# Kernel optimization log

Hardware: AMD Instinct MI355X
Metric: run time of the kernel (lower is better)

## Reference

```python
import jax, jax.numpy as jnp
import numpy as np
import math

B, T = 2, 1024
D_MODEL = 1024
N_HEAD = 16
HEAD_DIM = D_MODEL // N_HEAD
VOCAB = 32000
NUM_LOOP = 4
EPS_LN = 1e-5                       # torch LayerNorm default
EPS_RMS = float(np.finfo(np.float32).eps)  # torch RMSNorm eps=None -> finfo eps


def setup_inputs() -> dict:
    key = jax.random.key(0)
    ks = jax.random.split(key, 12)
    s = 0.02
    d = D_MODEL
    tok = jax.random.normal(ks[1], (VOCAB, d), jnp.float32) * s
    tok = tok.at[0].set(0.0)  # padding_idx=0
    return {
        "idx": jax.random.randint(ks[0], (B, T), 0, VOCAB),
        "tok_embed": tok,
        "ln_e_g": jnp.ones((d,), jnp.float32),
        "ln_e_b": jnp.zeros((d,), jnp.float32),
        "Wqkv": jax.random.normal(ks[2], (d, 3 * d), jnp.float32) * s,
        "bqkv": jnp.zeros((3 * d,), jnp.float32),
        "Wo": jax.random.normal(ks[3], (d, d), jnp.float32) * s,
        "bo": jnp.zeros((d,), jnp.float32),
        "W1": jax.random.normal(ks[4], (d, 4 * d), jnp.float32) * s,
        "b1": jnp.zeros((4 * d,), jnp.float32),
        "W2": jax.random.normal(ks[5], (4 * d, d), jnp.float32) * s,
        "b2": jnp.zeros((d,), jnp.float32),
        "n1_w": jnp.ones((d,), jnp.float32),
        "n2_w": jnp.ones((d,), jnp.float32),
        "lnf_g": jnp.ones((d,), jnp.float32),
        "lnf_b": jnp.zeros((d,), jnp.float32),
        "Wlm": jax.random.normal(ks[6], (d, VOCAB), jnp.float32) * s,
        "blm": jnp.zeros((VOCAB,), jnp.float32),
    }


def layernorm(x, g, b):
    m = jnp.mean(x, axis=-1, keepdims=True)
    v = jnp.mean(jnp.square(x - m), axis=-1, keepdims=True)
    return (x - m) * jax.lax.rsqrt(v + EPS_LN) * g + b


def rmsnorm(x, w):
    ms = jnp.mean(jnp.square(x), axis=-1, keepdims=True)
    return x * jax.lax.rsqrt(ms + EPS_RMS) * w


def gelu_tanh(x):
    c = math.sqrt(2.0 / math.pi)
    return 0.5 * x * (1.0 + jnp.tanh(c * (x + 0.044715 * x * x * x)))


def alibi_causal_bias(t):
    # rpe[q,k] = -(q-k) for q>k else 0, scaled per head by 2^(-8/H*(h+1)); causal -inf above diag
    pos = jnp.arange(t)
    rel = pos[:, None] - pos[None, :]                      # [T,T] = q - k
    slopes = 2.0 ** (-8.0 / N_HEAD * jnp.arange(1, N_HEAD + 1, dtype=jnp.float32))
    bias = -slopes[:, None, None] * rel.astype(jnp.float32)  # [H,T,T]
    return jnp.where(rel[None] >= 0, bias, -jnp.inf)       # causal mask fused


def reference(idx, tok_embed, ln_e_g, ln_e_b, Wqkv, bqkv, Wo, bo,
              W1, b1, W2, b2, n1_w, n2_w, lnf_g, lnf_b, Wlm, blm):
    b, t = idx.shape
    x = layernorm(tok_embed[idx], ln_e_g, ln_e_b)          # rpe=True: no sinusoidal PE
    bias = alibi_causal_bias(t)                            # [H,T,T]
    scale = 1.0 / math.sqrt(HEAD_DIM)

    for _ in range(NUM_LOOP):
        # attention sublayer
        h = rmsnorm(x, n1_w)
        qkv = h @ Wqkv + bqkv
        q, k, v = jnp.split(qkv, 3, axis=-1)
        q = q.reshape(b, t, N_HEAD, HEAD_DIM).transpose(0, 2, 1, 3)
        k = k.reshape(b, t, N_HEAD, HEAD_DIM).transpose(0, 2, 1, 3)
        v = v.reshape(b, t, N_HEAD, HEAD_DIM).transpose(0, 2, 1, 3)
        att = jnp.einsum('bhqd,bhkd->bhqk', q, k) * scale + bias[None]
        att = jax.nn.softmax(att, axis=-1)
        y = jnp.einsum('bhqk,bhkd->bhqd', att, v)
        y = y.transpose(0, 2, 1, 3).reshape(b, t, D_MODEL)
        x = x + (y @ Wo + bo)
        # mlp sublayer
        h = rmsnorm(x, n2_w)
        x = x + (gelu_tanh(h @ W1 + b1) @ W2 + b2)

    x = layernorm(x, lnf_g, lnf_b)
    return x @ Wlm + blm  # [B,T,VOCAB]
```

## Files before the change

### kernel.cpp

```cpp
#include <hip/hip_runtime.h>
#include <stdint.h>

#define DEVI __device__ __forceinline__

typedef __attribute__((ext_vector_type(8))) short short8;
typedef __attribute__((ext_vector_type(4))) float f32x4;
typedef unsigned short u16;
typedef unsigned int u32;

typedef const __attribute__((address_space(1))) void* gas_ptr;
typedef __attribute__((address_space(3))) void* las_ptr;

constexpr int BBATCH = 2;
constexpr int TT  = 1024;
constexpr int BT  = BBATCH * TT;
constexpr int DM  = 1024;
constexpr int NH  = 16;
constexpr int HD  = 64;
constexpr int DFF = 4096;
constexpr int NV  = 32000;
constexpr int NL  = 4;

DEVI u16 f2b(float f) {
  u32 u = __builtin_bit_cast(u32, f);
  u = (u + 0x7fffu + ((u >> 16) & 1u)) >> 16;
  return (u16)u;
}
DEVI float b2f(u16 h) { return __builtin_bit_cast(float, (u32)h << 16); }

DEVI void gld16(const void* g, void* l) {
  __builtin_amdgcn_global_load_lds((gas_ptr)g, (las_ptr)l, 16, 0, 0);
}

DEVI float wave_sum(float v) {
#pragma unroll
  for (int off = 32; off; off >>= 1) v += __shfl_xor(v, off);
  return v;
}
DEVI float block_sum(float v, float* sb) {
  v = wave_sum(v);
  int lane = threadIdx.x & 63, wid = threadIdx.x >> 6;
  __syncthreads();
  if (lane == 0) sb[wid] = v;
  __syncthreads();
  return sb[0] + sb[1] + sb[2] + sb[3];
}

DEVI float gelu_f(float x) {
  float u = 0.7978845608028654f * (x + 0.044715f * x * x * x);
  float e = __expf(2.0f * u);
  return x * (1.0f - 1.0f / (e + 1.0f));
}

__global__ __launch_bounds__(256) void wt_transpose_all(
    const float* __restrict__ Wqkv, const float* __restrict__ Wo,
    const float* __restrict__ W1, const float* __restrict__ W2,
    const float* __restrict__ Wlm,
    u16* __restrict__ WqkvT, u16* __restrict__ WoT, u16* __restrict__ W1T,
    u16* __restrict__ W2T, u16* __restrict__ WlmT) {
  __shared__ float t[32][33];
  int bid = blockIdx.x;
  const float* in; u16* out; int K, N, tt;
  if (bid < 3072)       { in = Wqkv; out = WqkvT; K = 1024; N = 3072;  tt = bid; }
  else if (bid < 4096)  { in = Wo;   out = WoT;   K = 1024; N = 1024;  tt = bid - 3072; }
  else if (bid < 8192)  { in = W1;   out = W1T;   K = 1024; N = 4096;  tt = bid - 4096; }
  else if (bid < 12288) { in = W2;   out = W2T;   K = 4096; N = 1024;  tt = bid - 8192; }
  else                  { in = Wlm;  out = WlmT;  K = 1024; N = 32000; tt = bid - 12288; }
  int nx = N >> 5;
  int n0 = (tt % nx) * 32, k0 = (tt / nx) * 32;
  int tx = threadIdx.x & 31, ty = threadIdx.x >> 5;
#pragma unroll
  for (int i = 0; i < 4; ++i)
    t[ty + 8 * i][tx] = in[(size_t)(k0 + ty + 8 * i) * N + n0 + tx];
  __syncthreads();
#pragma unroll
  for (int i = 0; i < 4; ++i)
    out[(size_t)(n0 + ty + 8 * i) * K + k0 + tx] = f2b(t[tx][ty + 8 * i]);
}

__global__ __launch_bounds__(256) void embed_ln_k(const int* __restrict__ idx,
                                                  const float* __restrict__ tok,
                                                  const float* __restrict__ g,
                                                  const float* __restrict__ b,
                                                  float* __restrict__ x) {
  __shared__ float sb[4];
  int row = blockIdx.x, tid = threadIdx.x;
  float4 v = ((const float4*)(tok + (size_t)idx[row] * DM))[tid];
  float s = block_sum(v.x + v.y + v.z + v.w, sb);
  float m = s * (1.0f / DM);
  float dx = v.x - m, dy = v.y - m, dz = v.z - m, dw = v.w - m;
  float q = block_sum(dx * dx + dy * dy + dz * dz + dw * dw, sb);
  float rs = rsqrtf(q * (1.0f / DM) + 1e-5f);
  float4 gg = ((const float4*)g)[tid];
  float4 bb = ((const float4*)b)[tid];
  float4 o = make_float4(dx * rs * gg.x + bb.x, dy * rs * gg.y + bb.y,
                         dz * rs * gg.z + bb.z, dw * rs * gg.w + bb.w);
  ((float4*)(x + (size_t)row * DM))[tid] = o;
}

__global__ __launch_bounds__(256) void final_ln_k(const float* __restrict__ x,
                                                  const float* __restrict__ g,
                                                  const float* __restrict__ b,
                                                  u16* __restrict__ xf) {
  __shared__ float sb[4];
  int row = blockIdx.x, tid = threadIdx.x;
  float4 v = ((const float4*)(x + (size_t)row * DM))[tid];
  float s = block_sum(v.x + v.y + v.z + v.w, sb);
  float m = s * (1.0f / DM);
  float dx = v.x - m, dy = v.y - m, dz = v.z - m, dw = v.w - m;
  float q = block_sum(dx * dx + dy * dy + dz * dz + dw * dw, sb);
  float rs = rsqrtf(q * (1.0f / DM) + 1e-5f);
  float4 gg = ((const float4*)g)[tid];
  float4 bb = ((const float4*)b)[tid];
  u32 lo = (u32)f2b(dx * rs * gg.x + bb.x) | ((u32)f2b(dy * rs * gg.y + bb.y) << 16);
  u32 hi = (u32)f2b(dz * rs * gg.z + bb.z) | ((u32)f2b(dw * rs * gg.w + bb.w) << 16);
  ((uint2*)(xf + (size_t)row * DM))[tid] = make_uint2(lo, hi);
}

__global__ __launch_bounds__(256) void rmsnorm_k(const float* __restrict__ x,
                                                 const float* __restrict__ w,
                                                 u16* __restrict__ h) {
  __shared__ float sb[4];
  int row = blockIdx.x, tid = threadIdx.x;
  float4 v = ((const float4*)(x + (size_t)row * DM))[tid];
  float q = block_sum(v.x * v.x + v.y * v.y + v.z * v.z + v.w * v.w, sb);
  float rs = rsqrtf(q * (1.0f / DM) + 1.1920928955078125e-7f);
  float4 ww = ((const float4*)w)[tid];
  u32 lo = (u32)f2b(v.x * rs * ww.x) | ((u32)f2b(v.y * rs * ww.y) << 16);
  u32 hi = (u32)f2b(v.z * rs * ww.z) | ((u32)f2b(v.w * rs * ww.w) << 16);
  ((uint2*)(h + (size_t)row * DM))[tid] = make_uint2(lo, hi);
}

__global__ __launch_bounds__(256) void attn_k(const u16* __restrict__ qkv,
                                              const u16* __restrict__ vT,
                                              u16* __restrict__ y) {
  __shared__ __align__(16) char sP[16384];
  __shared__ __align__(16) char sK[16384];
  __shared__ __align__(16) char sV[16384];
  const int tid = threadIdx.x, lane = tid & 63, wid = tid >> 6;
  const int bid = blockIdx.x;
  const int sl = (bid + (bid >> 8)) & 15;
  const int qt = (sl & 1) ? (sl >> 1) : (15 - (sl >> 1));
  const int bh = (bid >> 4) & 31, b = bh >> 4, h = bh & 15;
  const int nt = (qt >> 1) + 1;
  const float slope = exp2f(-0.5f * (float)(h + 1));

  const char* Qb = (const char*)(qkv + (size_t)b * TT * 3 * DM + h * HD);
  const char* Kb = (const char*)(qkv + (size_t)b * TT * 3 * DM + DM + h * HD);
  const char* Vb = (const char*)(vT + (size_t)bh * HD * TT);

#pragma unroll
  for (int ci = 0; ci < 2; ++ci) {
    int c = wid * 2 + ci;
    int r = c * 8 + (lane >> 3);
    int q = (lane & 7) ^ (r & 7);
    gld16(Qb + (size_t)(qt * 64 + r) * 6144 + q * 16, sP + c * 1024 + lane * 16);
  }

  auto stageKV = [&](int kt) {
    int kv0 = kt * 128;
#pragma unroll
    for (int ci = 0; ci < 4; ++ci) {
      int c = wid * 4 + ci;
      int r = c * 8 + (lane >> 3);
      int q = (lane & 7) ^ (r & 7);
      gld16(Kb + (size_t)(kv0 + r) * 6144 + q * 16, sK + c * 1024 + lane * 16);
    }
#pragma unroll
    for (int ci = 0; ci < 4; ++ci) {
      int c = wid * 4 + ci;
      int d = c * 4 + (lane >> 4);
      int q = (lane & 15) ^ (d & 15);
      gld16(Vb + (size_t)d * 2048 + (size_t)kv0 * 2 + q * 16, sV + c * 1024 + lane * 16);
    }
  };
  stageKV(0);
  asm volatile("s_waitcnt vmcnt(8)" ::: "memory");

  short8 qf[2];
#pragma unroll
  for (int ks = 0; ks < 2; ++ks) {
    int r = wid * 16 + (lane & 15);
    int q = ((ks << 2) + (lane >> 4)) ^ (r & 7);
    qf[ks] = *(const short8*)(sP + r * 128 + q * 16);
  }

  f32x4 Y[4] = {};
  float m_r[4], l_r[4];
#pragma unroll
  for (int r = 0; r < 4; ++r) { m_r[r] = -3e38f; l_r[r] = 0.0f; }

  for (int kt = 0; kt < nt; ++kt) {
    asm volatile("s_waitcnt vmcnt(0)" ::: "memory");
    __syncthreads();

    f32x4 s[8] = {};
    __builtin_amdgcn_s_setprio(1);
#pragma unroll
    for (int ks = 0; ks < 2; ++ks) {
      short8 kf[8];
#pragma unroll
      for (int j = 0; j < 8; ++j) {
        int r = j * 16 + (lane & 15);
        int q = ((ks << 2) + (lane >> 4)) ^ (r & 7);
        kf[j] = *(const short8*)(sK + r * 128 + q * 16);
      }
#pragma unroll
      for (int j = 0; j < 8; ++j)
        s[j] = __builtin_amdgcn_mfma_f32_16x16x32_bf16(qf[ks], kf[j], s[j], 0, 0, 0);
    }
    __builtin_amdgcn_s_setprio(0);

    const int kv0 = kt * 128;
    const int qbase = qt * 64 + wid * 16 + ((lane >> 4) << 2);
    float rowmax[4] = {-3e38f, -3e38f, -3e38f, -3e38f};
#pragma unroll
    for (int j = 0; j < 8; ++j) {
      int kcol = kv0 + j * 16 + (lane & 15);
#pragma unroll
      for (int r = 0; r < 4; ++r) {
        int qrow = qbase + r;
        float v = (kcol <= qrow) ? s[j][r] * 0.125f - slope * (float)(qrow - kcol) : -3e38f;
        s[j][r] = v;
        rowmax[r] = fmaxf(rowmax[r], v);
      }
    }
#pragma unroll
    for (int r = 0; r < 4; ++r) {
      rowmax[r] = fmaxf(rowmax[r], __shfl_xor(rowmax[r], 1));
      rowmax[r] = fmaxf(rowmax[r], __shfl_xor(rowmax[r], 2));
      rowmax[r] = fmaxf(rowmax[r], __shfl_xor(rowmax[r], 4));
      rowmax[r] = fmaxf(rowmax[r], __shfl_xor(rowmax[r], 8));
      float mn = fmaxf(m_r[r], rowmax[r]);
      float al = __expf(m_r[r] - mn);
      m_r[r] = mn;
      l_r[r] *= al;
#pragma unroll
      for (int j = 0; j < 4; ++j) Y[j][r] *= al;
    }
    float rs[4] = {0.0f, 0.0f, 0.0f, 0.0f};
#pragma unroll
    for (int j = 0; j < 8; ++j)
#pragma unroll
      for (int r = 0; r < 4; ++r) {
        float p = __expf(s[j][r] - m_r[r]);
        s[j][r] = p;
        rs[r] += p;
      }
#pragma unroll
    for (int r = 0; r < 4; ++r) {
      rs[r] += __shfl_xor(rs[r], 1);
      rs[r] += __shfl_xor(rs[r], 2);
      rs[r] += __shfl_xor(rs[r], 4);
      rs[r] += __shfl_xor(rs[r], 8);
      l_r[r] += rs[r];
    }
#pragma unroll
    for (int j = 0; j < 8; ++j)
#pragma unroll
      for (int r = 0; r < 4; ++r) {
        int rl = wid * 16 + ((lane >> 4) << 2) + r;
        int c = j * 16 + (lane & 15);
        int g = c >> 3;
        *(u16*)(sP + rl * 256 + ((g ^ (rl & 15)) << 4) + (c & 7) * 2) = f2b(s[j][r]);
      }

    __builtin_amdgcn_s_setprio(1);
#pragma unroll
    for (int ks = 0; ks < 4; ++ks) {
      short8 pf, vf[4];
      {
        int r = wid * 16 + (lane & 15);
        int q = ((ks << 2) + (lane >> 4)) ^ (r & 15);
        pf = *(const short8*)(sP + r * 256 + (q << 4));
      }
#pragma unroll
      for (int j = 0; j < 4; ++j) {
        int d = j * 16 + (lane & 15);
        int q = ((ks << 2) + (lane >> 4)) ^ (d & 15);
        vf[j] = *(const short8*)(sV + d * 256 + (q << 4));
      }
#pragma unroll
      for (int j = 0; j < 4; ++j)
        Y[j] = __builtin_amdgcn_mfma_f32_16x16x32_bf16(pf, vf[j], Y[j], 0, 0, 0);
    }
    __builtin_amdgcn_s_setprio(0);
    __syncthreads();
    if (kt + 1 < nt) stageKV(kt + 1);
  }

#pragma unroll
  for (int r = 0; r < 4; ++r) {
    float inv = 1.0f / l_r[r];
    int qrow = qt * 64 + wid * 16 + ((lane >> 4) << 2) + r;
    u16* yp = y + (size_t)(b * TT + qrow) * DM + h * HD;
#pragma unroll
    for (int j = 0; j < 4; ++j)
      yp[j * 16 + (lane & 15)] = f2b(Y[j][r] * inv);
  }
}

enum { EPI_BF16 = 0, EPI_GELU = 1, EPI_ADDF32 = 2, EPI_F32 = 3, EPI_ATOMIC = 4, EPI_QKV = 5 };

template <int BM, int BN, int WM, int WN, int EPI, int KS = 1>
__global__ __launch_bounds__(256, 2) void gemm_bt(
    const u16* __restrict__ A, int lda, const u16* __restrict__ Bt, int ldb,
    const float* __restrict__ bias, void* __restrict__ C, int ldc,
    float* __restrict__ resid, int K, u16* __restrict__ vTout) {
  constexpr int BK = 64;
  constexpr int NW = WM * WN;
  constexpr int FM = BM / WM / 16, FN = BN / WN / 16;
  constexpr int ABYTES = BM * BK * 2, BBYTES = BN * BK * 2;
  constexpr int ACH = ABYTES / 1024, BCH = BBYTES / 1024, NCH = ACH + BCH;
  extern __shared__ __align__(16) char smem[];

  const int tid = threadIdx.x, lane = tid & 63, wid = tid >> 6;
  const int brow = blockIdx.y * BM, bcol = blockIdx.x * BN;
  const long long kbase2 = (long long)blockIdx.z * (K / KS) * 2;

  const int nt = (K / KS) >> 6;
  const int widm = wid / WN, widn = wid % WN;
  const int rm0 = widm * (BM / WM), cn0 = widn * (BN / WN);

  f32x4 acc[FM][FN] = {};

  const int swq16 = (((lane & 7) ^ ((lane >> 3) & 7)) << 4);
  const int lrow8 = lane >> 3;

  auto stage = [&](int buf, int kt) {
    char* base = smem + buf * (ABYTES + BBYTES);
    const char* Ag = (const char*)A;
    const char* Bg = (const char*)Bt;
    long long kOff = kbase2 + (long long)kt * 128 + swq16;
#pragma unroll
    for (int ci = 0; ci < NCH / NW; ++ci) {
      int c = wid + ci * NW;
      if (c < ACH) {
        int r = c * 8 + lrow8;
        gld16(Ag + (long long)(brow + r) * (lda * 2) + kOff, base + c * 1024 + lane * 16);
      } else {
        int r = (c - ACH) * 8 + lrow8;
        gld16(Bg + (long long)(bcol + r) * (ldb * 2) + kOff,
              base + ABYTES + (c - ACH) * 1024 + lane * 16);
      }
    }
  };

  auto compute = [&](int buf) {
    char* baseA = smem + buf * (ABYTES + BBYTES);
    char* baseB = baseA + ABYTES;
#pragma unroll
    for (int ks = 0; ks < 2; ++ks) {
      short8 af[FM], bv[FN];
#pragma unroll
      for (int i = 0; i < FM; ++i) {
        int r = rm0 + i * 16 + (lane & 15);
        int cq = ((ks << 2) + (lane >> 4)) ^ (r & 7);
        af[i] = *(const short8*)(baseA + r * 128 + (cq << 4));
      }
#pragma unroll
      for (int j = 0; j < FN; ++j) {
        int r = cn0 + j * 16 + (lane & 15);
        int cq = ((ks << 2) + (lane >> 4)) ^ (r & 7);
        bv[j] = *(const short8*)(baseB + r * 128 + (cq << 4));
      }
#pragma unroll
      for (int i = 0; i < FM; ++i)
#pragma unroll
        for (int j = 0; j < FN; ++j)
          acc[i][j] = __builtin_amdgcn_mfma_f32_16x16x32_bf16(af[i], bv[j], acc[i][j], 0, 0, 0);
    }
  };

  stage(0, 0);
  __syncthreads();
  int cur = 0;
  for (int t = 0; t < nt; ++t) {
    if (t + 1 < nt) stage(cur ^ 1, t + 1);
    compute(cur);
    __syncthreads();
    cur ^= 1;
  }

  if constexpr (EPI == EPI_QKV) {
    if (bcol >= 2 * DM) {
      u16* st = (u16*)smem;
#pragma unroll
      for (int i = 0; i < FM; ++i)
#pragma unroll
        for (int j = 0; j < FN; ++j)
#pragma unroll
          for (int r = 0; r < 4; ++r) {
            int rl = rm0 + i * 16 + ((lane >> 4) << 2) + r;
            int cl = cn0 + j * 16 + (lane & 15);
            st[rl * 130 + cl] = f2b(acc[i][j][r] + bias[bcol + cl]);
          }
      __syncthreads();
      const int b = brow >> 10, t0b = brow & (TT - 1);
      const int h0 = (bcol - 2 * DM) >> 6;
      const int sub = tid & 15;
#pragma unroll
      for (int pass = 0; pass < 8; ++pass) {
        int d = pass * 16 + (tid >> 4);
        u32 pk[4];
#pragma unroll
        for (int k2 = 0; k2 < 4; ++k2) {
          u16 lo = st[(sub * 8 + 2 * k2) * 130 + d];
          u16 hi = st[(sub * 8 + 2 * k2 + 1) * 130 + d];
          pk[k2] = (u32)lo | ((u32)hi << 16);
        }
        int head = h0 + (d >> 6), dd = d & 63;
        *(uint4*)(vTout + ((size_t)((b * NH + head) * HD + dd)) * TT + t0b + sub * 8) =
            make_uint4(pk[0], pk[1], pk[2], pk[3]);
      }
      return;
    }
  }

  const int r0 = brow + rm0 + ((lane >> 4) << 2);
  const int c0 = bcol + cn0 + (lane & 15);
#pragma unroll
  for (int i = 0; i < FM; ++i) {
#pragma unroll
    for (int j = 0; j < FN; ++j) {
#pragma unroll
      for (int r = 0; r < 4; ++r) {
        int row = r0 + i * 16 + r;
        int col = c0 + j * 16;
        float v = acc[i][j][r];
        if constexpr (EPI == EPI_BF16 || EPI == EPI_QKV) {
          ((u16*)C)[(size_t)row * ldc + col] = f2b(v + bias[col]);
        } else if constexpr (EPI == EPI_GELU) {
          ((u16*)C)[(size_t)row * ldc + col] = f2b(gelu_f(v + bias[col]));
        } else if constexpr (EPI == EPI_ADDF32) {
          size_t o = (size_t)row * ldc + col;
          resid[o] += v + bias[col];
        } else if constexpr (EPI == EPI_ATOMIC) {
          size_t o = (size_t)row * ldc + col;
          atomicAdd(&resid[o], v + (blockIdx.z == 0 ? bias[col] : 0.0f));
        } else {
          ((float*)C)[(size_t)row * ldc + col] = v + bias[col];
        }
      }
    }
  }
}

template <int EPI>
__global__ __launch_bounds__(512, 2) void gemm8(
    const u16* __restrict__ A, int lda, const u16* __restrict__ Bt, int ldb,
    const float* __restrict__ bias, void* __restrict__ C, int ldc, int K, int nby) {
  __shared__ __align__(16) char smem[2][2][32768];
  const int tid = threadIdx.x, lane = tid & 63;
  const int wid = tid >> 6, wm = wid >> 2, wn = wid & 3;

  const int nb = gridDim.x;
  const int q8 = nb >> 3, r8 = nb & 7;
  const int xcd = blockIdx.x & 7, lin = blockIdx.x >> 3;
  const int idx = (xcd < r8 ? xcd * (q8 + 1) : r8 * (q8 + 1) + (xcd - r8) * q8) + lin;
  const int brow = (idx % nby) * 256, bcol = (idx / nby) * 256;

  const int nt = K >> 6, niter = nt >> 1;

  const int srow = tid >> 3, sq = tid & 7;
  auto stage = [&](int buf, int isB, int half, int kt) {
    const u16* G = isB ? Bt : A;
    const int ld = isB ? ldb : lda;
    const int base = isB ? bcol : brow;
    char* L = &smem[buf][isB][half * 16384];
#pragma unroll
    for (int l = 0; l < 2; ++l) {
      int rl = half * 128 + l * 64 + srow;
      gld16((const char*)G + (size_t)(base + rl) * (ld * 2) + kt * 128 + ((sq ^ (rl & 7)) << 4),
            L + l * 8192 + tid * 16);
    }
  };

  short8 bfr[4][2], afr[2][2];
  f32x4 acc[8][4] = {};

  stage(0, 0, 0, 0); stage(0, 0, 1, 0);
  stage(0, 1, 0, 0); stage(0, 1, 1, 0);
  stage(1, 1, 0, 1); stage(1, 1, 1, 1);
  asm volatile("s_waitcnt vmcnt(0)" ::: "memory");
  __builtin_amdgcn_s_barrier();

  for (int i = 0; i < niter; ++i) {
    const bool full = (i + 1 < niter);
    const int t2 = 2 * i + 2, t3 = 2 * i + 3;
#pragma unroll
    for (int h = 0; h < 2; ++h) {
#pragma unroll
      for (int qd = 0; qd < 4; ++qd) {
        if (qd == 0) {
#pragma unroll
          for (int j = 0; j < 4; ++j)
#pragma unroll
            for (int ks = 0; ks < 2; ++ks) {
              int r = wn * 64 + j * 16 + (lane & 15);
              int q = ((ks << 2) + (lane >> 4)) ^ (r & 7);
              bfr[j][ks] = *(const short8*)&smem[h][1][r * 128 + q * 16];
            }
        }
#pragma unroll
        for (int f = 0; f < 2; ++f)
#pragma unroll
          for (int ks = 0; ks < 2; ++ks) {
            int r = wm * 128 + (qd * 2 + f) * 16 + (lane & 15);
            int q = ((ks << 2) + (lane >> 4)) ^ (r & 7);
            afr[f][ks] = *(const short8*)&smem[h][0][r * 128 + q * 16];
          }
        if (h == 0) {
          if (qd == 0) stage(1, 0, 0, 2 * i + 1);
          else if (qd == 1) stage(1, 0, 1, 2 * i + 1);
          else if (qd == 2) { if (full) stage(0, 1, 0, t2); }
          else              { if (full) stage(0, 1, 1, t2); }
        } else {
          if (qd == 0)      { if (full) stage(0, 0, 0, t2); }
          else if (qd == 1) { if (full) stage(0, 0, 1, t2); }
          else if (qd == 2) { if (full) stage(1, 1, 0, t3); }
          else              { if (full) stage(1, 1, 1, t3); }
        }
        if (qd == 3) {
          if (full) asm volatile("s_waitcnt vmcnt(4)" ::: "memory");
          else if (h == 0) asm volatile("s_waitcnt vmcnt(0)" ::: "memory");
        }
        __builtin_amdgcn_s_barrier();
        asm volatile("s_waitcnt lgkmcnt(0)" ::: "memory");
        __builtin_amdgcn_s_setprio(1);
#pragma unroll
        for (int f = 0; f < 2; ++f)
#pragma unroll
          for (int j = 0; j < 4; ++j)
#pragma unroll
            for (int ks = 0; ks < 2; ++ks)
              acc[qd * 2 + f][j] = __builtin_amdgcn_mfma_f32_16x16x32_bf16(
                  afr[f][ks], bfr[j][ks], acc[qd * 2 + f][j], 0, 0, 0);
        __builtin_amdgcn_s_setprio(0);
        __builtin_amdgcn_s_barrier();
      }
    }
  }

  if constexpr (EPI == EPI_F32) {
    char* sf = &smem[0][0][0];
    float* C32 = (float*)C;
#pragma unroll
    for (int half = 0; half < 2; ++half) {
      if (wm == half) {
#pragma unroll
        for (int fi = 0; fi < 8; ++fi)
#pragma unroll
          for (int j = 0; j < 4; ++j) {
            int cl = wn * 64 + j * 16 + (lane & 15);
            float bv = bias[bcol + cl];
            int qsw = (cl >> 2);
#pragma unroll
            for (int r = 0; r < 4; ++r) {
              int row = fi * 16 + ((lane >> 4) << 2) + r;
              *(float*)(sf + row * 1024 + ((qsw ^ (row & 7)) << 4) + (cl & 3) * 4) =
                  acc[fi][j][r] + bv;
            }
          }
      }
      __syncthreads();
#pragma unroll
      for (int pass = 0; pass < 16; ++pass) {
        int row = pass * 8 + wid;
        float4 v4 = *(float4*)(sf + row * 1024 + ((lane ^ (row & 7)) << 4));
        *(float4*)(C32 + (size_t)(brow + half * 128 + row) * ldc + bcol + lane * 4) = v4;
      }
      __syncthreads();
    }
    return;
  }

  const int r0 = brow + wm * 128 + ((lane >> 4) << 2);
  const int c0 = bcol + wn * 64 + (lane & 15);
#pragma unroll
  for (int fi = 0; fi < 8; ++fi) {
#pragma unroll
    for (int j = 0; j < 4; ++j) {
      int col = c0 + j * 16;
      float bv = bias[col];
#pragma unroll
      for (int r = 0; r < 4; ++r) {
        int row = r0 + fi * 16 + r;
        float v = acc[fi][j][r] + bv;
        if constexpr (EPI == EPI_GELU)
          ((u16*)C)[(size_t)row * ldc + col] = f2b(gelu_f(v));
        else
          ((u16*)C)[(size_t)row * ldc + col] = f2b(v);
      }
    }
  }
}

extern "C" void kernel_launch(void* const* d_in, const int* in_sizes, int n_in,
                              void* d_out, int out_size, void* d_ws, size_t ws_size,
                              hipStream_t stream) {
  (void)in_sizes; (void)n_in; (void)out_size;
  const int*   idx    = (const int*)d_in[0];
  const float* tok    = (const float*)d_in[1];
  const float* ln_e_g = (const float*)d_in[2];
  const float* ln_e_b = (const float*)d_in[3];
  const float* Wqkv   = (const float*)d_in[4];
  const float* bqkv   = (const float*)d_in[5];
  const float* Wo     = (const float*)d_in[6];
  const float* bo     = (const float*)d_in[7];
  const float* W1     = (const float*)d_in[8];
  const float* b1     = (const float*)d_in[9];
  const float* W2     = (const float*)d_in[10];
  const float* b2     = (const float*)d_in[11];
  const float* n1_w   = (const float*)d_in[12];
  const float* n2_w   = (const float*)d_in[13];
  const float* lnf_g  = (const float*)d_in[14];
  const float* lnf_b  = (const float*)d_in[15];
  const float* Wlm    = (const float*)d_in[16];
  const float* blm    = (const float*)d_in[17];
  float* out = (float*)d_out;

  char* w = (char*)d_ws;
  auto alloc = [&](size_t bytes) { char* p = w; w += (bytes + 255) & ~(size_t)255; return p; };
  float* x   = (float*)alloc((size_t)BT * DM * 4);
  u16* h     = (u16*)alloc((size_t)BT * DM * 2);
  u16* qkv   = (u16*)alloc((size_t)BT * 3 * DM * 2);
  u16* vT    = (u16*)alloc((size_t)BBATCH * NH * HD * TT * 2);
  u16* y     = (u16*)alloc((size_t)BT * DM * 2);
  u16* act   = (u16*)alloc((size_t)BT * DFF * 2);
  u16* xf    = (u16*)alloc((size_t)BT * DM * 2);
  u16* WqkvT = (u16*)alloc((size_t)3 * DM * DM * 2);
  u16* WoT   = (u16*)alloc((size_t)DM * DM * 2);
  u16* W1T   = (u16*)alloc((size_t)DFF * DM * 2);
  u16* W2T   = (u16*)alloc((size_t)DM * DFF * 2);
  u16* WlmT  = (u16*)alloc((size_t)NV * DM * 2);
  if ((size_t)(w - (char*)d_ws) > ws_size) return;

  wt_transpose_all<<<44288, 256, 0, stream>>>(Wqkv, Wo, W1, W2, Wlm,
                                              WqkvT, WoT, W1T, W2T, WlmT);

  embed_ln_k<<<BT, 256, 0, stream>>>(idx, tok, ln_e_g, ln_e_b, x);

  constexpr int SM128 = 2 * (128 * 64 * 2 + 128 * 64 * 2);
  constexpr int SM64  = 2 * (128 * 64 * 2 + 64 * 64 * 2);

  for (int l = 0; l < NL; ++l) {
    rmsnorm_k<<<BT, 256, 0, stream>>>(x, n1_w, h);
    gemm_bt<128, 128, 2, 2, EPI_QKV><<<dim3(3 * DM / 128, BT / 128), 256, SM128, stream>>>(
        h, DM, WqkvT, DM, bqkv, qkv, 3 * DM, nullptr, DM, vT);
    attn_k<<<512, 256, 0, stream>>>(qkv, vT, y);
    gemm_bt<128, 64, 4, 1, EPI_ATOMIC, 2><<<dim3(DM / 64, BT / 128, 2), 256, SM64, stream>>>(
        y, DM, WoT, DM, bo, nullptr, DM, x, DM, nullptr);
    rmsnorm_k<<<BT, 256, 0, stream>>>(x, n2_w, h);
    gemm_bt<128, 128, 2, 2, EPI_GELU><<<dim3(DFF / 128, BT / 128), 256, SM128, stream>>>(
        h, DM, W1T, DM, b1, act, DFF, nullptr, DM, nullptr);
    gemm_bt<128, 128, 2, 2, EPI_ATOMIC, 4><<<dim3(DM / 128, BT / 128, 4), 256, SM128, stream>>>(
        act, DFF, W2T, DFF, b2, nullptr, DM, x, DFF, nullptr);
  }

  final_ln_k<<<BT, 256, 0, stream>>>(x, lnf_g, lnf_b, xf);
  gemm8<EPI_F32><<<dim3((NV / 256) * (BT / 256)), 512, 0, stream>>>(
      xf, DM, WlmT, DM, blm, out, NV, DM, BT / 256);
}
```

Baseline: 851.5 us.

## Add 128x256 eight-wave GEMM for W1, widen weight transpose tiles, simplify F32 epilogue

Adds a new gemm8n kernel: 512 threads, 128x256 tiles, double-buffered LDS and XCD-aware block remapping. It replaces the 128x128 gemm_bt for the W1+GELU projection, aiming for more data reuse and better occupancy per block. The weight transpose kernel now handles 64x32 tiles and writes packed 32-bit bf16 pairs, which halves its block count and widens its stores. The LDS-staged coalesced F32 epilogue in gemm8 is replaced by direct strided scalar stores. That could slow the large LM-head output write.

```diff
diff --git a/kernel.cpp b/kernel.cpp
--- a/kernel.cpp
+++ b/kernel.cpp
@@ -58,24 +58,27 @@
     const float* __restrict__ Wlm,
     u16* __restrict__ WqkvT, u16* __restrict__ WoT, u16* __restrict__ W1T,
     u16* __restrict__ W2T, u16* __restrict__ WlmT) {
-  __shared__ float t[32][33];
+  __shared__ float t[64][33];
   int bid = blockIdx.x;
   const float* in; u16* out; int K, N, tt;
-  if (bid < 3072)       { in = Wqkv; out = WqkvT; K = 1024; N = 3072;  tt = bid; }
-  else if (bid < 4096)  { in = Wo;   out = WoT;   K = 1024; N = 1024;  tt = bid - 3072; }
-  else if (bid < 8192)  { in = W1;   out = W1T;   K = 1024; N = 4096;  tt = bid - 4096; }
-  else if (bid < 12288) { in = W2;   out = W2T;   K = 4096; N = 1024;  tt = bid - 8192; }
-  else                  { in = Wlm;  out = WlmT;  K = 1024; N = 32000; tt = bid - 12288; }
+  if (bid < 1536)      { in = Wqkv; out = WqkvT; K = 1024; N = 3072;  tt = bid; }
+  else if (bid < 2048) { in = Wo;   out = WoT;   K = 1024; N = 1024;  tt = bid - 1536; }
+  else if (bid < 4096) { in = W1;   out = W1T;   K = 1024; N = 4096;  tt = bid - 2048; }
+  else if (bid < 6144) { in = W2;   out = W2T;   K = 4096; N = 1024;  tt = bid - 4096; }
+  else                 { in = Wlm;  out = WlmT;  K = 1024; N = 32000; tt = bid - 6144; }
   int nx = N >> 5;
-  int n0 = (tt % nx) * 32, k0 = (tt / nx) * 32;
+  int n0 = (tt % nx) * 32, k0 = (tt / nx) * 64;
   int tx = threadIdx.x & 31, ty = threadIdx.x >> 5;
 #pragma unroll
-  for (int i = 0; i < 4; ++i)
+  for (int i = 0; i < 8; ++i)
     t[ty + 8 * i][tx] = in[(size_t)(k0 + ty + 8 * i) * N + n0 + tx];
   __syncthreads();
 #pragma unroll
-  for (int i = 0; i < 4; ++i)
-    out[(size_t)(n0 + ty + 8 * i) * K + k0 + tx] = f2b(t[tx][ty + 8 * i]);
+  for (int i = 0; i < 4; ++i) {
+    int r = ty + 8 * i;
+    u32 pk = (u32)f2b(t[2 * tx][r]) | ((u32)f2b(t[2 * tx + 1][r]) << 16);
+    *(u32*)(out + (size_t)(n0 + r) * K + k0 + 2 * tx) = pk;
+  }
 }
 
 __global__ __launch_bounds__(256) void embed_ln_k(const int* __restrict__ idx,
@@ -542,39 +545,6 @@
     }
   }
 
-  if constexpr (EPI == EPI_F32) {
-    char* sf = &smem[0][0][0];
-    float* C32 = (float*)C;
-#pragma unroll
-    for (int half = 0; half < 2; ++half) {
-      if (wm == half) {
-#pragma unroll
-        for (int fi = 0; fi < 8; ++fi)
-#pragma unroll
-          for (int j = 0; j < 4; ++j) {
-            int cl = wn * 64 + j * 16 + (lane & 15);
-            float bv = bias[bcol + cl];
-            int qsw = (cl >> 2);
-#pragma unroll
-            for (int r = 0; r < 4; ++r) {
-              int row = fi * 16 + ((lane >> 4) << 2) + r;
-              *(float*)(sf + row * 1024 + ((qsw ^ (row & 7)) << 4) + (cl & 3) * 4) =
-                  acc[fi][j][r] + bv;
-            }
-          }
-      }
-      __syncthreads();
-#pragma unroll
-      for (int pass = 0; pass < 16; ++pass) {
-        int row = pass * 8 + wid;
-        float4 v4 = *(float4*)(sf + row * 1024 + ((lane ^ (row & 7)) << 4));
-        *(float4*)(C32 + (size_t)(brow + half * 128 + row) * ldc + bcol + lane * 4) = v4;
-      }
-      __syncthreads();
-    }
-    return;
-  }
-
   const int r0 = brow + wm * 128 + ((lane >> 4) << 2);
   const int c0 = bcol + wn * 64 + (lane & 15);
 #pragma unroll
@@ -587,7 +557,126 @@
       for (int r = 0; r < 4; ++r) {
         int row = r0 + fi * 16 + r;
         float v = acc[fi][j][r] + bv;
-        if constexpr (EPI == EPI_GELU)
+        if constexpr (EPI == EPI_F32)
+          ((float*)C)[(size_t)row * ldc + col] = v;
+        else if constexpr (EPI == EPI_GELU)
+          ((u16*)C)[(size_t)row * ldc + col] = f2b(gelu_f(v));
+        else
+          ((u16*)C)[(size_t)row * ldc + col] = f2b(v);
+      }
+    }
+  }
+}
+
+template <int EPI>
+__global__ __launch_bounds__(512, 2) void gemm8n(
+    const u16* __restrict__ A, int lda, const u16* __restrict__ Bt, int ldb,
+    const float* __restrict__ bias, void* __restrict__ C, int ldc, int K, int nby) {
+  __shared__ __align__(16) char sA[2][16384];
+  __shared__ __align__(16) char sB[2][32768];
+  const int tid = threadIdx.x, lane = tid & 63;
+  const int wid = tid >> 6, wm = wid >> 2, wn = wid & 3;
+
+  const int nb = gridDim.x;
+  const int q8 = nb >> 3, r8 = nb & 7;
+  const int xcd = blockIdx.x & 7, lin = blockIdx.x >> 3;
+  const int idx = (xcd < r8 ? xcd * (q8 + 1) : r8 * (q8 + 1) + (xcd - r8) * q8) + lin;
+  const int brow = (idx % nby) * 128, bcol = (idx / nby) * 256;
+
+  const int nt = K >> 6, niter = nt >> 1;
+
+  const int srow = tid >> 3, sq = tid & 7;
+  auto stageA = [&](int buf, int half, int kt) {
+    int rl = half * 64 + srow;
+    gld16((const char*)A + (size_t)(brow + rl) * (lda * 2) + kt * 128 + ((sq ^ (rl & 7)) << 4),
+          sA[buf] + half * 8192 + tid * 16);
+  };
+  auto stageB = [&](int buf, int half, int kt) {
+#pragma unroll
+    for (int l = 0; l < 2; ++l) {
+      int rl = half * 128 + l * 64 + srow;
+      gld16((const char*)Bt + (size_t)(bcol + rl) * (ldb * 2) + kt * 128 + ((sq ^ (rl & 7)) << 4),
+            sB[buf] + half * 16384 + l * 8192 + tid * 16);
+    }
+  };
+
+  short8 bfr[4][2], afr[2];
+  f32x4 acc[4][4] = {};
+
+  stageA(0, 0, 0); stageA(0, 1, 0);
+  stageB(0, 0, 0); stageB(0, 1, 0);
+  stageB(1, 0, 1); stageB(1, 1, 1);
+  asm volatile("s_waitcnt vmcnt(0)" ::: "memory");
+  __builtin_amdgcn_s_barrier();
+
+  for (int i = 0; i < niter; ++i) {
+    const bool full = (i + 1 < niter);
+    const int t2 = 2 * i + 2, t3 = 2 * i + 3;
+#pragma unroll
+    for (int h = 0; h < 2; ++h) {
+#pragma unroll
+      for (int qd = 0; qd < 4; ++qd) {
+        if (qd == 0) {
+#pragma unroll
+          for (int j = 0; j < 4; ++j)
+#pragma unroll
+            for (int ks = 0; ks < 2; ++ks) {
+              int r = wn * 64 + j * 16 + (lane & 15);
+              int q = ((ks << 2) + (lane >> 4)) ^ (r & 7);
+              bfr[j][ks] = *(const short8*)&sB[h][r * 128 + q * 16];
+            }
+        }
+#pragma unroll
+        for (int ks = 0; ks < 2; ++ks) {
+          int r = wm * 64 + qd * 16 + (lane & 15);
+          int q = ((ks << 2) + (lane >> 4)) ^ (r & 7);
+          afr[ks] = *(const short8*)&sA[h][r * 128 + q * 16];
+        }
+        if (h == 0) {
+          if (qd == 0) stageA(1, 0, 2 * i + 1);
+          else if (qd == 1) stageA(1, 1, 2 * i + 1);
+          else if (qd == 2) { if (full) stageB(0, 0, t2); }
+          else              { if (full) stageB(0, 1, t2); }
+        } else {
+          if (qd == 0)      { if (full) stageA(0, 0, t2); }
+          else if (qd == 1) { if (full) stageA(0, 1, t2); }
+          else if (qd == 2) { if (full) stageB(1, 0, t3); }
+          else              { if (full) stageB(1, 1, t3); }
+        }
+        if (qd == 3) {
+          if (full) asm volatile("s_waitcnt vmcnt(4)" ::: "memory");
+          else if (h == 0) asm volatile("s_waitcnt vmcnt(0)" ::: "memory");
+        }
+        __builtin_amdgcn_s_barrier();
+        asm volatile("s_waitcnt lgkmcnt(0)" ::: "memory");
+        __builtin_amdgcn_s_setprio(1);
+#pragma unroll
+        for (int j = 0; j < 4; ++j)
+#pragma unroll
+          for (int ks = 0; ks < 2; ++ks)
+            acc[qd][j] = __builtin_amdgcn_mfma_f32_16x16x32_bf16(
+                afr[ks], bfr[j][ks], acc[qd][j], 0, 0, 0);
+        __builtin_amdgcn_s_setprio(0);
+        __builtin_amdgcn_s_barrier();
+      }
+    }
+  }
+
+  const int r0 = brow + wm * 64 + ((lane >> 4) << 2);
+  const int c0 = bcol + wn * 64 + (lane & 15);
+#pragma unroll
+  for (int fi = 0; fi < 4; ++fi) {
+#pragma unroll
+    for (int j = 0; j < 4; ++j) {
+      int col = c0 + j * 16;
+      float bv = bias[col];
+#pragma unroll
+      for (int r = 0; r < 4; ++r) {
+        int row = r0 + fi * 16 + r;
+        float v = acc[fi][j][r] + bv;
+        if constexpr (EPI == EPI_F32)
+          ((float*)C)[(size_t)row * ldc + col] = v;
+        else if constexpr (EPI == EPI_GELU)
           ((u16*)C)[(size_t)row * ldc + col] = f2b(gelu_f(v));
         else
           ((u16*)C)[(size_t)row * ldc + col] = f2b(v);
@@ -636,7 +725,7 @@
   u16* WlmT  = (u16*)alloc((size_t)NV * DM * 2);
   if ((size_t)(w - (char*)d_ws) > ws_size) return;
 
-  wt_transpose_all<<<44288, 256, 0, stream>>>(Wqkv, Wo, W1, W2, Wlm,
+  wt_transpose_all<<<22144, 256, 0, stream>>>(Wqkv, Wo, W1, W2, Wlm,
                                               WqkvT, WoT, W1T, W2T, WlmT);
 
   embed_ln_k<<<BT, 256, 0, stream>>>(idx, tok, ln_e_g, ln_e_b, x);
@@ -652,8 +741,8 @@
     gemm_bt<128, 64, 4, 1, EPI_ATOMIC, 2><<<dim3(DM / 64, BT / 128, 2), 256, SM64, stream>>>(
         y, DM, WoT, DM, bo, nullptr, DM, x, DM, nullptr);
     rmsnorm_k<<<BT, 256, 0, stream>>>(x, n2_w, h);
-    gemm_bt<128, 128, 2, 2, EPI_GELU><<<dim3(DFF / 128, BT / 128), 256, SM128, stream>>>(
-        h, DM, W1T, DM, b1, act, DFF, nullptr, DM, nullptr);
+    gemm8n<EPI_GELU><<<dim3((BT / 128) * (DFF / 256)), 512, 0, stream>>>(
+        h, DM, W1T, DM, b1, act, DFF, DM, BT / 128);
     gemm_bt<128, 128, 2, 2, EPI_ATOMIC, 4><<<dim3(DM / 128, BT / 128, 4), 256, SM128, stream>>>(
         act, DFF, W2T, DFF, b2, nullptr, DM, x, DFF, nullptr);
   }
```

Result: no change. 859.5 us (+0.9%).

## Widen weight transpose tiles, shrink QKV GEMM tile, drop LDS-staged f32 epilogue

Applied to the files above, without the earlier changes.

The weight transpose kernel now handles 64x32 tiles per block and writes packed pairs of bf16 as 32-bit stores, halving the grid and widening global writes. The QKV GEMM switches to a 64-row tile so more blocks launch, and its V-transpose epilogue is generalized to the tile height. The LM-head GEMM's LDS-staged, swizzled fp32 epilogue is removed in favor of direct per-element global stores, which simplifies the code but likely produces poorly coalesced writes of the large logits output.

```diff
diff --git a/kernel.cpp b/kernel.cpp
--- a/kernel.cpp
+++ b/kernel.cpp
@@ -58,24 +58,27 @@
     const float* __restrict__ Wlm,
     u16* __restrict__ WqkvT, u16* __restrict__ WoT, u16* __restrict__ W1T,
     u16* __restrict__ W2T, u16* __restrict__ WlmT) {
-  __shared__ float t[32][33];
+  __shared__ float t[64][33];
   int bid = blockIdx.x;
   const float* in; u16* out; int K, N, tt;
-  if (bid < 3072)       { in = Wqkv; out = WqkvT; K = 1024; N = 3072;  tt = bid; }
-  else if (bid < 4096)  { in = Wo;   out = WoT;   K = 1024; N = 1024;  tt = bid - 3072; }
-  else if (bid < 8192)  { in = W1;   out = W1T;   K = 1024; N = 4096;  tt = bid - 4096; }
-  else if (bid < 12288) { in = W2;   out = W2T;   K = 4096; N = 1024;  tt = bid - 8192; }
-  else                  { in = Wlm;  out = WlmT;  K = 1024; N = 32000; tt = bid - 12288; }
+  if (bid < 1536)      { in = Wqkv; out = WqkvT; K = 1024; N = 3072;  tt = bid; }
+  else if (bid < 2048) { in = Wo;   out = WoT;   K = 1024; N = 1024;  tt = bid - 1536; }
+  else if (bid < 4096) { in = W1;   out = W1T;   K = 1024; N = 4096;  tt = bid - 2048; }
+  else if (bid < 6144) { in = W2;   out = W2T;   K = 4096; N = 1024;  tt = bid - 4096; }
+  else                 { in = Wlm;  out = WlmT;  K = 1024; N = 32000; tt = bid - 6144; }
   int nx = N >> 5;
-  int n0 = (tt % nx) * 32, k0 = (tt / nx) * 32;
+  int n0 = (tt % nx) * 32, k0 = (tt / nx) * 64;
   int tx = threadIdx.x & 31, ty = threadIdx.x >> 5;
 #pragma unroll
-  for (int i = 0; i < 4; ++i)
+  for (int i = 0; i < 8; ++i)
     t[ty + 8 * i][tx] = in[(size_t)(k0 + ty + 8 * i) * N + n0 + tx];
   __syncthreads();
 #pragma unroll
-  for (int i = 0; i < 4; ++i)
-    out[(size_t)(n0 + ty + 8 * i) * K + k0 + tx] = f2b(t[tx][ty + 8 * i]);
+  for (int i = 0; i < 4; ++i) {
+    int r = ty + 8 * i;
+    u32 pk = (u32)f2b(t[2 * tx][r]) | ((u32)f2b(t[2 * tx + 1][r]) << 16);
+    *(u32*)(out + (size_t)(n0 + r) * K + k0 + 2 * tx) = pk;
+  }
 }
 
 __global__ __launch_bounds__(256) void embed_ln_k(const int* __restrict__ idx,
@@ -398,10 +401,12 @@
       __syncthreads();
       const int b = brow >> 10, t0b = brow & (TT - 1);
       const int h0 = (bcol - 2 * DM) >> 6;
-      const int sub = tid & 15;
-#pragma unroll
-      for (int pass = 0; pass < 8; ++pass) {
-        int d = pass * 16 + (tid >> 4);
+      constexpr int NCHK = BM / 8;
+      constexpr int DPP = 256 / NCHK;
+      const int sub = tid & (NCHK - 1);
+#pragma unroll
+      for (int pass = 0; pass < 128 / DPP; ++pass) {
+        int d = pass * DPP + (tid / NCHK);
         u32 pk[4];
 #pragma unroll
         for (int k2 = 0; k2 < 4; ++k2) {
@@ -542,39 +547,6 @@
     }
   }
 
-  if constexpr (EPI == EPI_F32) {
-    char* sf = &smem[0][0][0];
-    float* C32 = (float*)C;
-#pragma unroll
-    for (int half = 0; half < 2; ++half) {
-      if (wm == half) {
-#pragma unroll
-        for (int fi = 0; fi < 8; ++fi)
-#pragma unroll
-          for (int j = 0; j < 4; ++j) {
-            int cl = wn * 64 + j * 16 + (lane & 15);
-            float bv = bias[bcol + cl];
-            int qsw = (cl >> 2);
-#pragma unroll
-            for (int r = 0; r < 4; ++r) {
-              int row = fi * 16 + ((lane >> 4) << 2) + r;
-              *(float*)(sf + row * 1024 + ((qsw ^ (row & 7)) << 4) + (cl & 3) * 4) =
-                  acc[fi][j][r] + bv;
-            }
-          }
-      }
-      __syncthreads();
-#pragma unroll
-      for (int pass = 0; pass < 16; ++pass) {
-        int row = pass * 8 + wid;
-        float4 v4 = *(float4*)(sf + row * 1024 + ((lane ^ (row & 7)) << 4));
-        *(float4*)(C32 + (size_t)(brow + half * 128 + row) * ldc + bcol + lane * 4) = v4;
-      }
-      __syncthreads();
-    }
-    return;
-  }
-
   const int r0 = brow + wm * 128 + ((lane >> 4) << 2);
   const int c0 = bcol + wn * 64 + (lane & 15);
 #pragma unroll
@@ -587,7 +559,9 @@
       for (int r = 0; r < 4; ++r) {
         int row = r0 + fi * 16 + r;
         float v = acc[fi][j][r] + bv;
-        if constexpr (EPI == EPI_GELU)
+        if constexpr (EPI == EPI_F32)
+          ((float*)C)[(size_t)row * ldc + col] = v;
+        else if constexpr (EPI == EPI_GELU)
           ((u16*)C)[(size_t)row * ldc + col] = f2b(gelu_f(v));
         else
           ((u16*)C)[(size_t)row * ldc + col] = f2b(v);
@@ -636,17 +610,18 @@
   u16* WlmT  = (u16*)alloc((size_t)NV * DM * 2);
   if ((size_t)(w - (char*)d_ws) > ws_size) return;
 
-  wt_transpose_all<<<44288, 256, 0, stream>>>(Wqkv, Wo, W1, W2, Wlm,
+  wt_transpose_all<<<22144, 256, 0, stream>>>(Wqkv, Wo, W1, W2, Wlm,
                                               WqkvT, WoT, W1T, W2T, WlmT);
 
   embed_ln_k<<<BT, 256, 0, stream>>>(idx, tok, ln_e_g, ln_e_b, x);
 
   constexpr int SM128 = 2 * (128 * 64 * 2 + 128 * 64 * 2);
   constexpr int SM64  = 2 * (128 * 64 * 2 + 64 * 64 * 2);
+  constexpr int SMQ   = 2 * (64 * 64 * 2 + 128 * 64 * 2);
 
   for (int l = 0; l < NL; ++l) {
     rmsnorm_k<<<BT, 256, 0, stream>>>(x, n1_w, h);
-    gemm_bt<128, 128, 2, 2, EPI_QKV><<<dim3(3 * DM / 128, BT / 128), 256, SM128, stream>>>(
+    gemm_bt<64, 128, 2, 2, EPI_QKV><<<dim3(3 * DM / 128, BT / 64), 256, SMQ, stream>>>(
         h, DM, WqkvT, DM, bqkv, qkv, 3 * DM, nullptr, DM, vT);
     attn_k<<<512, 256, 0, stream>>>(qkv, vT, y);
     gemm_bt<128, 64, 4, 1, EPI_ATOMIC, 2><<<dim3(DM / 64, BT / 128, 2), 256, SM64, stream>>>(
```

New measurement: 842.8 us. About the same (-1.0%).
